# Kernel tuning notes

Measured on AMD Instinct MI355X. Metric: run time of the kernel, lower is better.

Reference implementation:

```python
import jax, jax.numpy as jnp
import numpy as np

T, H = 4096, 2048


def setup_inputs() -> dict:
    key = jax.random.key(0)
    k_a, k_b, k_x = jax.random.split(key, 3)
    # glorot-style init matching the module: uniform(-1,1) * sqrt(2/sum(shape))
    a = jax.random.uniform(k_a, (H,), minval=-1.0, maxval=1.0) * jnp.sqrt(2.0 / H)
    B = jax.random.uniform(k_b, (H, H), minval=-1.0, maxval=1.0) * jnp.sqrt(2.0 / (2 * H))
    x = jax.random.normal(k_x, (T, H), dtype=jnp.float32)
    return {"x": x, "a": a, "B": B}


def reference(x, a, B):
    # x: (T, H); per-timestep s_t = B.T @ x_t  ->  s = x @ B, laid out NCH = (1, H, T)
    Tl, Hl = x.shape
    s = jnp.einsum("th,hk->kt", x, B)[None]  # (1, H, T)
    # depthwise causal kernel: k[h, t] = a[h]**t, time as final dim, flipped for conv
    exponents = jnp.arange(Tl)
    kernel = jnp.power(a[:, None], exponents)          # (H, T)
    kernel_flipped = jnp.flip(kernel, axis=-1)[:, None, :]  # (H, 1, T) OIH
    s_padded = jnp.pad(s, ((0, 0), (0, 0), (Tl - 1, 0)))    # causal left-pad
    conv_out = jax.lax.conv_general_dilated(
        s_padded, kernel_flipped,
        window_strides=(1,), padding="VALID",
        dimension_numbers=("NCH", "OIH", "NCH"),
        feature_group_count=Hl,
    )  # (1, H, T): h_t[h] = sum_{k<=t} a[h]**(t-k) * s_k[h]
    return jnp.transpose(conv_out, (0, 2, 1))  # (1, T, H)
```

## Files before the change

kernel.cpp:

```cpp
#include <hip/hip_runtime.h>
#include <stdint.h>

#define TDIM 4096
#define HDIM 2048

#define BM 128
#define BN 128
#define BK 64
#define NKT (HDIM / BK)
#define AREG  18432
#define PERBUF 34816
#define SSTR   132

typedef short short8 __attribute__((ext_vector_type(8)));
typedef float f32x4 __attribute__((ext_vector_type(4)));

__device__ __forceinline__ uint16_t f2bf(float f) {
  uint32_t u = __builtin_bit_cast(uint32_t, f);
  u += 0x7fffu + ((u >> 16) & 1u);
  return (uint16_t)(u >> 16);
}
__device__ __forceinline__ float bf2f(uint32_t h) {
  uint32_t u = h << 16;
  return __builtin_bit_cast(float, u);
}

__device__ __forceinline__ void async_copy16(const void* gsrc, void* ldst) {
  __builtin_amdgcn_global_load_lds(
      (const __attribute__((address_space(1))) uint32_t*)gsrc,
      (__attribute__((address_space(3))) uint32_t*)ldst,
      16, 0, 0);
}

__global__ void prep(const float* __restrict__ x, const float* __restrict__ B,
                     uint16_t* __restrict__ xb, uint16_t* __restrict__ Bt) {
  __shared__ uint16_t tile[64][68];
  const int t = threadIdx.x;
  if (blockIdx.x < 4096) {
    size_t i = ((size_t)blockIdx.x * 256 + t) * 8;
    float4 v0 = *(const float4*)(x + i);
    float4 v1 = *(const float4*)(x + i + 4);
    union { uint16_t h[8]; uint4 v; } o;
    o.h[0] = f2bf(v0.x); o.h[1] = f2bf(v0.y); o.h[2] = f2bf(v0.z); o.h[3] = f2bf(v0.w);
    o.h[4] = f2bf(v1.x); o.h[5] = f2bf(v1.y); o.h[6] = f2bf(v1.z); o.h[7] = f2bf(v1.w);
    *(uint4*)(xb + i) = o.v;
  } else {
    const int bid = blockIdx.x - 4096;
    const int n0 = (bid & 31) * 64;
    const int k0 = (bid >> 5) * 64;
    {
      const int r  = t >> 4;
      const int c4 = (t & 15) * 4;
#pragma unroll
      for (int i = 0; i < 4; ++i) {
        int rr = r + i * 16;
        float4 v = *(const float4*)&B[(size_t)(k0 + rr) * HDIM + n0 + c4];
        union { uint16_t h[4]; uint2 u; } o;
        o.h[0] = f2bf(v.x); o.h[1] = f2bf(v.y); o.h[2] = f2bf(v.z); o.h[3] = f2bf(v.w);
        *(uint2*)&tile[rr][c4] = o.u;
      }
    }
    __syncthreads();
    {
      const int nr = t >> 2;
      const int kc = (t & 3) * 4;
#pragma unroll
      for (int i = 0; i < 4; ++i) {
        int kk = kc + i * 16;
        union { uint16_t h[4]; uint2 u; } o;
        o.h[0] = tile[kk][nr];     o.h[1] = tile[kk + 1][nr];
        o.h[2] = tile[kk + 2][nr]; o.h[3] = tile[kk + 3][nr];
        *(uint2*)&Bt[(size_t)(n0 + nr) * HDIM + k0 + kk] = o.u;
      }
    }
  }
}

__global__ __launch_bounds__(256, 2) void gemm_scan(
    const uint16_t* __restrict__ A, const uint16_t* __restrict__ Bt,
    const float* __restrict__ a, float* __restrict__ out) {
  __shared__ __align__(16) char lds[2 * PERBUF];

  const int tid  = threadIdx.x;
  const int lane = tid & 63;
  const int wave = tid >> 6;
  const int wm = (wave >> 1) * 64;
  const int wn = (wave & 1) * 64;
  const int m0 = blockIdx.y * BM;
  const int n0 = blockIdx.x * BN;

  f32x4 acc[4][4] = {};
  f32x4 accw[4] = {};

  const int lr = lane >> 3;
  const int gc = (lane & 7) ^ lr;

  const int fr = lane & 15;
  const int fq = lane >> 4;

  auto issue_tile = [&](int kt2) {
    size_t koff = (size_t)kt2 * (BK * 2);
    char* dst = lds + (kt2 & 1) * PERBUF;
#pragma unroll
    for (int i = 0; i < 4; ++i) {
      int g = wave * 4 + i;
      int row = m0 - 16 + g * 8 + lr;
      if (row < 0) row = 0;
      async_copy16((const char*)A + ((size_t)row * HDIM + gc * 8) * 2 + koff,
                   dst + g * 1024);
    }
    if (wave < 2) {
      int g = 16 + wave;
      int row = m0 - 16 + g * 8 + lr;
      async_copy16((const char*)A + ((size_t)row * HDIM + gc * 8) * 2 + koff,
                   dst + g * 1024);
    }
#pragma unroll
    for (int i = 0; i < 4; ++i) {
      int g = wave * 4 + i;
      int row = n0 + g * 8 + lr;
      async_copy16((const char*)Bt + ((size_t)row * HDIM + gc * 8) * 2 + koff,
                   dst + AREG + g * 1024);
    }
  };

  issue_tile(0);
  for (int kt = 0; kt < NKT; ++kt) {
    if (kt + 1 < NKT) {
      issue_tile(kt + 1);
      if (wave < 2) asm volatile("s_waitcnt vmcnt(9)" ::: "memory");
      else          asm volatile("s_waitcnt vmcnt(8)" ::: "memory");
    } else {
      asm volatile("s_waitcnt vmcnt(0)" ::: "memory");
    }
    asm volatile("s_barrier" ::: "memory");

    const char* base = lds + (kt & 1) * PERBUF;
#pragma unroll
    for (int s = 0; s < 2; ++s) {
      short8 af[4], bfr[4], aw;
#pragma unroll
      for (int im = 0; im < 4; ++im) {
        int row = 16 + wm + im * 16 + fr;
        af[im] = *(const short8*)(base + row * 128 + (((s * 4 + fq) ^ (fr & 7)) * 16));
      }
#pragma unroll
      for (int in = 0; in < 4; ++in) {
        int row = wn + in * 16 + fr;
        bfr[in] = *(const short8*)(base + AREG + row * 128 + (((s * 4 + fq) ^ (fr & 7)) * 16));
      }
#pragma unroll
      for (int im = 0; im < 4; ++im)
#pragma unroll
        for (int in = 0; in < 4; ++in)
          acc[im][in] = __builtin_amdgcn_mfma_f32_16x16x32_bf16(
              af[im], bfr[in], acc[im][in], 0, 0, 0);
      if (wave < 2) {
        aw = *(const short8*)(base + fr * 128 + (((s * 4 + fq) ^ (fr & 7)) * 16));
#pragma unroll
        for (int in = 0; in < 4; ++in)
          accw[in] = __builtin_amdgcn_mfma_f32_16x16x32_bf16(
              aw, bfr[in], accw[in], 0, 0, 0);
      }
    }

    asm volatile("s_barrier" ::: "memory");
  }

  uint16_t* Sl = (uint16_t*)lds;
#pragma unroll
  for (int im = 0; im < 4; ++im)
#pragma unroll
    for (int in = 0; in < 4; ++in)
#pragma unroll
      for (int r = 0; r < 4; ++r)
        Sl[(16 + wm + im * 16 + fq * 4 + r) * SSTR + wn + in * 16 + fr] =
            f2bf(acc[im][in][r]);
  if (wave < 2) {
#pragma unroll
    for (int in = 0; in < 4; ++in)
#pragma unroll
      for (int r = 0; r < 4; ++r)
        Sl[(fq * 4 + r) * SSTR + wn + in * 16 + fr] = f2bf(accw[in][r]);
  }
  __syncthreads();

  const int col   = tid & 127;
  const int chunk = tid >> 7;
  const float av  = a[n0 + col];
  float h = 0.f;
  if (!(m0 == 0 && chunk == 0)) {
#pragma unroll
    for (int i = 0; i < 16; ++i)
      h = av * h + bf2f(Sl[(chunk * 64 + i) * SSTR + col]);
  }
  float* op = out + (size_t)(m0 + chunk * 64) * HDIM + n0 + col;
#pragma unroll
  for (int i = 0; i < 64; ++i) {
    h = av * h + bf2f(Sl[(chunk * 64 + 16 + i) * SSTR + col]);
    op[(size_t)i * HDIM] = h;
  }
}

extern "C" void kernel_launch(void* const* d_in, const int* in_sizes, int n_in,
                              void* d_out, int out_size, void* d_ws, size_t ws_size,
                              hipStream_t stream) {
  const float* x = (const float*)d_in[0];
  const float* a = (const float*)d_in[1];
  const float* B = (const float*)d_in[2];
  float* out = (float*)d_out;

  uint16_t* xb  = (uint16_t*)d_ws;
  uint16_t* Btb = (uint16_t*)((char*)d_ws + (size_t)16 * 1024 * 1024);

  prep<<<4096 + 1024, 256, 0, stream>>>(x, B, xb, Btb);
  gemm_scan<<<dim3(HDIM / BN, TDIM / BM), 256, 0, stream>>>(xb, Btb, a, out);
}
```

Baseline: 138.7 us.

## Split K across two wave groups with 512-thread blocks and LDS reduction

```diff
diff --git a/kernel.cpp b/kernel.cpp
--- a/kernel.cpp
+++ b/kernel.cpp
@@ -76,7 +76,7 @@
   }
 }
 
-__global__ __launch_bounds__(256, 2) void gemm_scan(
+__global__ __launch_bounds__(512, 4) void gemm_scan(
     const uint16_t* __restrict__ A, const uint16_t* __restrict__ Bt,
     const float* __restrict__ a, float* __restrict__ out) {
   __shared__ __align__(16) char lds[2 * PERBUF];
@@ -84,28 +84,34 @@
   const int tid  = threadIdx.x;
   const int lane = tid & 63;
   const int wave = tid >> 6;
-  const int wm = (wave >> 1) * 64;
-  const int wn = (wave & 1) * 64;
+  const int kg   = wave >> 2;
+  const int wq   = wave & 3;
+  const int wm = (wq >> 1) * 64;
+  const int wn = (wq & 1) * 64;
   const int m0 = blockIdx.y * BM;
   const int n0 = blockIdx.x * BN;
 
   f32x4 acc[4][4] = {};
-  f32x4 accw[4] = {};
+  f32x4 accw[2] = {};
 
   const int lr = lane >> 3;
   const int gc = (lane & 7) ^ lr;
 
   const int fr = lane & 15;
   const int fq = lane >> 4;
+  const int iw0 = (wq >> 1) * 2;
 
   auto issue_tile = [&](int kt2) {
     size_t koff = (size_t)kt2 * (BK * 2);
     char* dst = lds + (kt2 & 1) * PERBUF;
-#pragma unroll
-    for (int i = 0; i < 4; ++i) {
-      int g = wave * 4 + i;
+    {
+      int g = wave;
       int row = m0 - 16 + g * 8 + lr;
       if (row < 0) row = 0;
+      async_copy16((const char*)A + ((size_t)row * HDIM + gc * 8) * 2 + koff,
+                   dst + g * 1024);
+      g = wave + 8;
+      row = m0 - 16 + g * 8 + lr;
       async_copy16((const char*)A + ((size_t)row * HDIM + gc * 8) * 2 + koff,
                    dst + g * 1024);
     }
@@ -116,8 +122,8 @@
                    dst + g * 1024);
     }
 #pragma unroll
-    for (int i = 0; i < 4; ++i) {
-      int g = wave * 4 + i;
+    for (int i = 0; i < 2; ++i) {
+      int g = wave + i * 8;
       int row = n0 + g * 8 + lr;
       async_copy16((const char*)Bt + ((size_t)row * HDIM + gc * 8) * 2 + koff,
                    dst + AREG + g * 1024);
@@ -128,60 +134,86 @@
   for (int kt = 0; kt < NKT; ++kt) {
     if (kt + 1 < NKT) {
       issue_tile(kt + 1);
-      if (wave < 2) asm volatile("s_waitcnt vmcnt(9)" ::: "memory");
-      else          asm volatile("s_waitcnt vmcnt(8)" ::: "memory");
+      if (wave < 2) asm volatile("s_waitcnt vmcnt(5)" ::: "memory");
+      else          asm volatile("s_waitcnt vmcnt(4)" ::: "memory");
     } else {
       asm volatile("s_waitcnt vmcnt(0)" ::: "memory");
     }
     asm volatile("s_barrier" ::: "memory");
 
     const char* base = lds + (kt & 1) * PERBUF;
-#pragma unroll
-    for (int s = 0; s < 2; ++s) {
-      short8 af[4], bfr[4], aw;
-#pragma unroll
-      for (int im = 0; im < 4; ++im) {
-        int row = 16 + wm + im * 16 + fr;
-        af[im] = *(const short8*)(base + row * 128 + (((s * 4 + fq) ^ (fr & 7)) * 16));
-      }
-#pragma unroll
-      for (int in = 0; in < 4; ++in) {
-        int row = wn + in * 16 + fr;
-        bfr[in] = *(const short8*)(base + AREG + row * 128 + (((s * 4 + fq) ^ (fr & 7)) * 16));
-      }
-#pragma unroll
-      for (int im = 0; im < 4; ++im)
-#pragma unroll
-        for (int in = 0; in < 4; ++in)
-          acc[im][in] = __builtin_amdgcn_mfma_f32_16x16x32_bf16(
-              af[im], bfr[in], acc[im][in], 0, 0, 0);
-      if (wave < 2) {
-        aw = *(const short8*)(base + fr * 128 + (((s * 4 + fq) ^ (fr & 7)) * 16));
-#pragma unroll
-        for (int in = 0; in < 4; ++in)
-          accw[in] = __builtin_amdgcn_mfma_f32_16x16x32_bf16(
-              aw, bfr[in], accw[in], 0, 0, 0);
-      }
-    }
+    const int coff = ((kg * 4 + fq) ^ (fr & 7)) * 16;
+    short8 af[4], bfr[4], aw;
+#pragma unroll
+    for (int im = 0; im < 4; ++im) {
+      int row = 16 + wm + im * 16 + fr;
+      af[im] = *(const short8*)(base + row * 128 + coff);
+    }
+#pragma unroll
+    for (int in = 0; in < 4; ++in) {
+      int row = wn + in * 16 + fr;
+      bfr[in] = *(const short8*)(base + AREG + row * 128 + coff);
+    }
+    aw = *(const short8*)(base + fr * 128 + coff);
+#pragma unroll
+    for (int im = 0; im < 4; ++im)
+#pragma unroll
+      for (int in = 0; in < 4; ++in)
+        acc[im][in] = __builtin_amdgcn_mfma_f32_16x16x32_bf16(
+            af[im], bfr[in], acc[im][in], 0, 0, 0);
+#pragma unroll
+    for (int iw = 0; iw < 2; ++iw)
+      accw[iw] = __builtin_amdgcn_mfma_f32_16x16x32_bf16(
+          aw, bfr[iw0 + iw], accw[iw], 0, 0, 0);
 
     asm volatile("s_barrier" ::: "memory");
   }
 
+  float* X = (float*)lds;
+  if (kg == 1) {
+#pragma unroll
+    for (int im = 0; im < 4; ++im)
+#pragma unroll
+      for (int in = 0; in < 4; ++in)
+        *(f32x4*)(X + wq * 4096 + (im * 4 + in) * 256 + lane * 4) = acc[im][in];
+  }
+  __syncthreads();
+  if (kg == 0) {
+#pragma unroll
+    for (int im = 0; im < 4; ++im)
+#pragma unroll
+      for (int in = 0; in < 4; ++in)
+        acc[im][in] += *(f32x4*)(X + wq * 4096 + (im * 4 + in) * 256 + lane * 4);
+  }
+  __syncthreads();
+  if (kg == 1) {
+#pragma unroll
+    for (int iw = 0; iw < 2; ++iw)
+      *(f32x4*)(X + wq * 512 + iw * 256 + lane * 4) = accw[iw];
+  }
+  __syncthreads();
+  if (kg == 0) {
+#pragma unroll
+    for (int iw = 0; iw < 2; ++iw)
+      accw[iw] += *(f32x4*)(X + wq * 512 + iw * 256 + lane * 4);
+  }
+  __syncthreads();
+
   uint16_t* Sl = (uint16_t*)lds;
-#pragma unroll
-  for (int im = 0; im < 4; ++im)
-#pragma unroll
-    for (int in = 0; in < 4; ++in)
+  if (kg == 0) {
+#pragma unroll
+    for (int im = 0; im < 4; ++im)
+#pragma unroll
+      for (int in = 0; in < 4; ++in)
+#pragma unroll
+        for (int r = 0; r < 4; ++r)
+          Sl[(16 + wm + im * 16 + fq * 4 + r) * SSTR + wn + in * 16 + fr] =
+              f2bf(acc[im][in][r]);
+#pragma unroll
+    for (int iw = 0; iw < 2; ++iw)
 #pragma unroll
       for (int r = 0; r < 4; ++r)
-        Sl[(16 + wm + im * 16 + fq * 4 + r) * SSTR + wn + in * 16 + fr] =
-            f2bf(acc[im][in][r]);
-  if (wave < 2) {
-#pragma unroll
-    for (int in = 0; in < 4; ++in)
-#pragma unroll
-      for (int r = 0; r < 4; ++r)
-        Sl[(fq * 4 + r) * SSTR + wn + in * 16 + fr] = f2bf(accw[in][r]);
+        Sl[(fq * 4 + r) * SSTR + wn + (iw0 + iw) * 16 + fr] = f2bf(accw[iw][r]);
   }
   __syncthreads();
 
@@ -192,12 +224,12 @@
   if (!(m0 == 0 && chunk == 0)) {
 #pragma unroll
     for (int i = 0; i < 16; ++i)
-      h = av * h + bf2f(Sl[(chunk * 64 + i) * SSTR + col]);
-  }
-  float* op = out + (size_t)(m0 + chunk * 64) * HDIM + n0 + col;
-#pragma unroll
-  for (int i = 0; i < 64; ++i) {
-    h = av * h + bf2f(Sl[(chunk * 64 + 16 + i) * SSTR + col]);
+      h = av * h + bf2f(Sl[(chunk * 32 + i) * SSTR + col]);
+  }
+  float* op = out + (size_t)(m0 + chunk * 32) * HDIM + n0 + col;
+#pragma unroll
+  for (int i = 0; i < 32; ++i) {
+    h = av * h + bf2f(Sl[(chunk * 32 + 16 + i) * SSTR + col]);
     op[(size_t)i * HDIM] = h;
   }
 }
@@ -214,5 +246,5 @@
   uint16_t* Btb = (uint16_t*)((char*)d_ws + (size_t)16 * 1024 * 1024);
 
   prep<<<4096 + 1024, 256, 0, stream>>>(x, B, xb, Btb);
-  gemm_scan<<<dim3(HDIM / BN, TDIM / BM), 256, 0, stream>>>(xb, Btb, a, out);
-}
+  gemm_scan<<<dim3(HDIM / BN, TDIM / BM), 512, 0, stream>>>(xb, Btb, a, out);
+}
```

Result: slower. 407.5 us (+193.7%).
